# Optimization experiments

Measured on AMD Instinct MI355X. Metric: run time of the kernel, lower is better.

The kernel has to match this reference:

```python
import jax, jax.numpy as jnp
import numpy as np

L, B, H, P = 2048, 16, 512, 256
EPS = 1e-6  # flax nnx LayerNorm default


def setup_inputs() -> dict:
    key = jax.random.key(0)
    ks = jax.random.split(key, 12)
    x = jax.random.normal(ks[0], (L, B, H), jnp.float32)
    d = jax.random.bernoulli(ks[1], 0.01, (L, B))  # sparse reset signal
    hidden_re = jnp.zeros((1, B, P), jnp.float32)
    hidden_im = jnp.zeros((1, B, P), jnp.float32)
    # S5 diagonal state matrix (stable: Re < 0)
    Lambda_re = -0.5 * jnp.exp(0.5 * jax.random.normal(ks[2], (P,), jnp.float32))
    Lambda_im = np.float32(np.pi) * jax.random.normal(ks[3], (P,), jnp.float32)
    B_re = jax.random.normal(ks[4], (P, H), jnp.float32) / np.sqrt(2.0 * H).astype(np.float32)
    B_im = jax.random.normal(ks[5], (P, H), jnp.float32) / np.sqrt(2.0 * H).astype(np.float32)
    C_re = jax.random.normal(ks[6], (H, P), jnp.float32) / np.sqrt(P).astype(np.float32)
    C_im = jax.random.normal(ks[7], (H, P), jnp.float32) / np.sqrt(P).astype(np.float32)
    D = jax.random.normal(ks[8], (H,), jnp.float32)
    log_step = jax.random.uniform(ks[9], (P,), jnp.float32,
                                  minval=np.log(1e-3).astype(np.float32),
                                  maxval=np.log(1e-1).astype(np.float32))
    ln_scale = jnp.ones((H,), jnp.float32)
    ln_bias = jnp.zeros((H,), jnp.float32)
    out2_w = jax.random.normal(ks[10], (H, H), jnp.float32) / np.sqrt(H).astype(np.float32)
    out2_b = jnp.zeros((H,), jnp.float32)
    return dict(x=x, d=d, hidden_re=hidden_re, hidden_im=hidden_im,
                Lambda_re=Lambda_re, Lambda_im=Lambda_im, B_re=B_re, B_im=B_im,
                C_re=C_re, C_im=C_im, D=D, log_step=log_step,
                ln_scale=ln_scale, ln_bias=ln_bias, out2_w=out2_w, out2_b=out2_b)


def reference(x, d, hidden_re, hidden_im, Lambda_re, Lambda_im, B_re, B_im,
              C_re, C_im, D, log_step, ln_scale, ln_bias, out2_w, out2_b):
    def ln(v):
        mu = v.mean(-1, keepdims=True)
        var = v.var(-1, keepdims=True)
        return (v - mu) * jax.lax.rsqrt(var + EPS) * ln_scale + ln_bias

    skip = x
    xn = ln(x)  # prenorm

    # --- S5 SSM (ZOH discretization), vmapped over batch == vectorized over axis 1 ---
    step = jnp.exp(log_step)  # step_rescale = 1.0
    Lam = (Lambda_re + 1j * Lambda_im).astype(jnp.complex64)          # (P,)
    Lam_bar = jnp.exp(Lam * step.astype(jnp.complex64))                # (P,)
    B_bar = ((Lam_bar - 1.0) / Lam)[:, None] * (B_re + 1j * B_im).astype(jnp.complex64)  # (P,H)
    Bu = jnp.einsum('lbh,ph->lbp', xn.astype(jnp.complex64), B_bar)    # (L,B,P)

    keep = (1.0 - d.astype(jnp.float32)).astype(jnp.complex64)         # reset zeroes the carry
    a = Lam_bar[None, None, :] * keep[:, :, None]                      # (L,B,P)
    h0 = (hidden_re + 1j * hidden_im).astype(jnp.complex64)[0]         # (B,P)
    Bu = Bu.at[0].add(a[0] * h0)                                       # fold in initial hidden

    def binop(e1, e2):
        a1, b1 = e1
        a2, b2 = e2
        return (a2 * a1, a2 * b1 + b2)

    _, xs = jax.lax.associative_scan(binop, (a, Bu), axis=0)           # (L,B,P) states
    Cmat = (C_re + 1j * C_im).astype(jnp.complex64)
    ys = 2.0 * jnp.einsum('lbp,hp->lbh', xs, Cmat).real + D * xn       # conj-sym readout + feedthrough
    new_hidden = xs[-1:]                                               # (1,B,P)

    y = ln(ys)  # gtrxl norm (shared LayerNorm)
    # half_glu2: x * sigmoid(W2 gelu(x) + b2)
    x1 = jax.nn.gelu(y)  # approximate=True matches nnx.gelu
    y = y * jax.nn.sigmoid(x1 @ out2_w + out2_b)
    out = skip + y
    return (new_hidden.real, new_hidden.imag, out)
```

## Files before the change

### kernel.cpp

```cpp
#include <hip/hip_runtime.h>

#define LL 2048
#define BB 16
#define HH 512
#define PP 256
#define MM (LL*BB)
#define NN 512
#define KK 512
#define NC 64
#define CLEN 32

typedef __bf16 bf16x8 __attribute__((ext_vector_type(8)));
typedef float  f32x4  __attribute__((ext_vector_type(4)));

__device__ __forceinline__ unsigned short f2bf(float f) {
  unsigned u = __builtin_bit_cast(unsigned, f);
  u = (u + 0x7fffu + ((u >> 16) & 1u)) >> 16;
  return (unsigned short)u;
}
__device__ __forceinline__ float bf2f(unsigned short s) {
  unsigned u = ((unsigned)s) << 16;
  return __builtin_bit_cast(float, u);
}

__global__ void detect_kernel(const unsigned int* __restrict__ dw, int* __restrict__ flag) {
  __shared__ int sInt, sFloat;
  if (threadIdx.x == 0) { sInt = 1; sFloat = 1; }
  __syncthreads();
  int allInt = 1, allFloat = 1;
  for (int i = threadIdx.x; i < 8192; i += 256) {
    unsigned v = dw[i];
    if (v > 1u) allInt = 0;
    if (v != 0u && v != 0x3f800000u) allFloat = 0;
  }
  if (!allInt) atomicAnd(&sInt, 0);
  if (!allFloat) atomicAnd(&sFloat, 0);
  __syncthreads();
  if (threadIdx.x == 0) *flag = sInt ? 0 : (sFloat ? 1 : 2);
}

__device__ __forceinline__ float keep_val(const void* d, int flag, int idx) {
  if (flag == 0) return 1.f - (float)((const int*)d)[idx];
  if (flag == 1) return 1.f - ((const float*)d)[idx];
  return 1.f - (float)((const unsigned char*)d)[idx];
}

__global__ void precompute_kernel(
    const float* __restrict__ Lre, const float* __restrict__ Lim,
    const float* __restrict__ Bre, const float* __restrict__ Bim,
    const float* __restrict__ Cre, const float* __restrict__ Cim,
    const float* __restrict__ lstep, const float* __restrict__ w2,
    unsigned short* __restrict__ W1t, unsigned short* __restrict__ W2t,
    unsigned short* __restrict__ W3t, float* __restrict__ lam_re,
    float* __restrict__ lam_im) {
  int t = blockIdx.x * 256 + threadIdx.x;
  int k = t & (KK - 1);
  int n = t >> 9;
  {
    int p = n & (PP - 1);
    float lr = Lre[p], li = Lim[p];
    float st = expf(lstep[p]);
    float er = expf(lr * st);
    float ang = li * st;
    float lbr = er * cosf(ang), lbi = er * sinf(ang);
    float den = lr * lr + li * li;
    float wr = ((lbr - 1.f) * lr + lbi * li) / den;
    float wi = (lbi * lr - (lbr - 1.f) * li) / den;
    float br = Bre[p * HH + k], bi = Bim[p * HH + k];
    float v = (n < PP) ? (wr * br - wi * bi) : (wr * bi + wi * br);
    W1t[(size_t)n * KK + k] = f2bf(v);
  }
  {
    float v = (k < PP) ? (2.f * Cre[n * PP + k]) : (-2.f * Cim[n * PP + (k - PP)]);
    W2t[(size_t)n * KK + k] = f2bf(v);
  }
  W3t[(size_t)n * KK + k] = f2bf(w2[(size_t)k * HH + n]);
  if (t < PP) {
    float lr = Lre[t], li = Lim[t];
    float st = expf(lstep[t]);
    float er = expf(lr * st);
    float ang = li * st;
    lam_re[t] = er * cosf(ang);
    lam_im[t] = er * sinf(ang);
  }
}

__global__ void ln1_kernel(const float* __restrict__ x, const float* __restrict__ sc,
                           const float* __restrict__ bs, unsigned short* __restrict__ xn) {
  int row = blockIdx.x * 4 + (threadIdx.x >> 6);
  int lane = threadIdx.x & 63;
  const float4* xr = (const float4*)(x + (size_t)row * HH) + lane * 2;
  float4 a = xr[0], b = xr[1];
  float s = (a.x + a.y) + (a.z + a.w) + (b.x + b.y) + (b.z + b.w);
  float q = a.x * a.x + a.y * a.y + a.z * a.z + a.w * a.w +
            b.x * b.x + b.y * b.y + b.z * b.z + b.w * b.w;
#pragma unroll
  for (int off = 32; off; off >>= 1) { s += __shfl_xor(s, off); q += __shfl_xor(q, off); }
  float mean = s * (1.f / HH);
  float var = fmaxf(q * (1.f / HH) - mean * mean, 0.f);
  float rstd = rsqrtf(var + 1e-6f);
  const float4* scp = (const float4*)sc + lane * 2;
  const float4* bsp = (const float4*)bs + lane * 2;
  float4 s0 = scp[0], s1 = scp[1], b0 = bsp[0], b1 = bsp[1];
  unsigned short o[8];
  o[0] = f2bf((a.x - mean) * rstd * s0.x + b0.x);
  o[1] = f2bf((a.y - mean) * rstd * s0.y + b0.y);
  o[2] = f2bf((a.z - mean) * rstd * s0.z + b0.z);
  o[3] = f2bf((a.w - mean) * rstd * s0.w + b0.w);
  o[4] = f2bf((b.x - mean) * rstd * s1.x + b1.x);
  o[5] = f2bf((b.y - mean) * rstd * s1.y + b1.y);
  o[6] = f2bf((b.z - mean) * rstd * s1.z + b1.z);
  o[7] = f2bf((b.w - mean) * rstd * s1.w + b1.w);
  uint4 pk;
  pk.x = o[0] | ((unsigned)o[1] << 16);
  pk.y = o[2] | ((unsigned)o[3] << 16);
  pk.z = o[4] | ((unsigned)o[5] << 16);
  pk.w = o[6] | ((unsigned)o[7] << 16);
  *((uint4*)(xn + (size_t)row * HH) + lane) = pk;
}

__global__ void ln2_kernel(const float* __restrict__ ys, const float* __restrict__ sc,
                           const float* __restrict__ bs, unsigned short* __restrict__ y,
                           unsigned short* __restrict__ x1) {
  int row = blockIdx.x * 4 + (threadIdx.x >> 6);
  int lane = threadIdx.x & 63;
  const float4* xr = (const float4*)(ys + (size_t)row * HH) + lane * 2;
  float4 a = xr[0], b = xr[1];
  float s = (a.x + a.y) + (a.z + a.w) + (b.x + b.y) + (b.z + b.w);
  float q = a.x * a.x + a.y * a.y + a.z * a.z + a.w * a.w +
            b.x * b.x + b.y * b.y + b.z * b.z + b.w * b.w;
#pragma unroll
  for (int off = 32; off; off >>= 1) { s += __shfl_xor(s, off); q += __shfl_xor(q, off); }
  float mean = s * (1.f / HH);
  float var = fmaxf(q * (1.f / HH) - mean * mean, 0.f);
  float rstd = rsqrtf(var + 1e-6f);
  const float4* scp = (const float4*)sc + lane * 2;
  const float4* bsp = (const float4*)bs + lane * 2;
  float4 s0 = scp[0], s1 = scp[1], b0 = bsp[0], b1 = bsp[1];
  float v[8] = { a.x, a.y, a.z, a.w, b.x, b.y, b.z, b.w };
  float scv[8] = { s0.x, s0.y, s0.z, s0.w, s1.x, s1.y, s1.z, s1.w };
  float bsv[8] = { b0.x, b0.y, b0.z, b0.w, b1.x, b1.y, b1.z, b1.w };
  unsigned short oy[8], og[8];
#pragma unroll
  for (int j = 0; j < 8; j++) {
    float yv = (v[j] - mean) * rstd * scv[j] + bsv[j];
    oy[j] = f2bf(yv);
    float g = 0.5f * yv * (1.f + tanhf(0.7978845608f * (yv + 0.044715f * yv * yv * yv)));
    og[j] = f2bf(g);
  }
  uint4 py, pg;
  py.x = oy[0] | ((unsigned)oy[1] << 16); py.y = oy[2] | ((unsigned)oy[3] << 16);
  py.z = oy[4] | ((unsigned)oy[5] << 16); py.w = oy[6] | ((unsigned)oy[7] << 16);
  pg.x = og[0] | ((unsigned)og[1] << 16); pg.y = og[2] | ((unsigned)og[3] << 16);
  pg.z = og[4] | ((unsigned)og[5] << 16); pg.w = og[6] | ((unsigned)og[7] << 16);
  *((uint4*)(y  + (size_t)row * HH) + lane) = py;
  *((uint4*)(x1 + (size_t)row * HH) + lane) = pg;
}

template <int EPI>
__global__ __launch_bounds__(256, 4) void gemm_kernel(
    const unsigned short* __restrict__ A, const unsigned short* __restrict__ Wt,
    float* __restrict__ Cout, const float* __restrict__ Dvec,
    const unsigned short* __restrict__ aux16, const float* __restrict__ skip) {
  __shared__ alignas(16) unsigned short lA[128 * 64];
  __shared__ alignas(16) unsigned short lB[128 * 64];
  int tid = threadIdx.x;
  int w = tid >> 6, lane = tid & 63;
  int wgid = blockIdx.x;
  int xcd = wgid & 7, idx = wgid >> 3;
  int m0 = (xcd * 32 + (idx >> 2)) * 128;
  int n0 = (idx & 3) * 128;
  int wr = w >> 1, wc = w & 1;
  f32x4 acc[4][4];
#pragma unroll
  for (int i = 0; i < 4; i++)
#pragma unroll
    for (int j = 0; j < 4; j++) acc[i][j] = (f32x4){0.f, 0.f, 0.f, 0.f};

  for (int kt = 0; kt < KK / 64; ++kt) {
    __syncthreads();
#pragma unroll
    for (int i = 0; i < 4; i++) {
      int sidx = i * 256 + tid;
      int r = sidx >> 3, c = sidx & 7;
      int cs = c ^ (r & 7);
      const unsigned short* g = A + (size_t)(m0 + r) * KK + kt * 64 + cs * 8;
      unsigned short* l = &lA[(i * 256 + w * 64) * 8];
      __builtin_amdgcn_global_load_lds((const __attribute__((address_space(1))) void*)g,
                                       (__attribute__((address_space(3))) void*)l, 16, 0, 0);
    }
#pragma unroll
    for (int i = 0; i < 4; i++) {
      int sidx = i * 256 + tid;
      int r = sidx >> 3, c = sidx & 7;
      int cs = c ^ (r & 7);
      const unsigned short* g = Wt + (size_t)(n0 + r) * KK + kt * 64 + cs * 8;
      unsigned short* l = &lB[(i * 256 + w * 64) * 8];
      __builtin_amdgcn_global_load_lds((const __attribute__((address_space(1))) void*)g,
                                       (__attribute__((address_space(3))) void*)l, 16, 0, 0);
    }
    __syncthreads();
#pragma unroll
    for (int ks = 0; ks < 2; ++ks) {
      bf16x8 aF[4], bF[4];
#pragma unroll
      for (int m = 0; m < 4; m++) {
        int row = wr * 64 + m * 16 + (lane & 15);
        int s = ks * 4 + (lane >> 4);
        aF[m] = *reinterpret_cast<const bf16x8*>(&lA[row * 64 + (s ^ (row & 7)) * 8]);
      }
#pragma unroll
      for (int n = 0; n < 4; n++) {
        int row = wc * 64 + n * 16 + (lane & 15);
        int s = ks * 4 + (lane >> 4);
        bF[n] = *reinterpret_cast<const bf16x8*>(&lB[row * 64 + (s ^ (row & 7)) * 8]);
      }
#pragma unroll
      for (int m = 0; m < 4; m++)
#pragma unroll
        for (int n = 0; n < 4; n++)
          acc[m][n] = __builtin_amdgcn_mfma_f32_16x16x32_bf16(aF[m], bF[n], acc[m][n], 0, 0, 0);
    }
  }
  int lr4 = (lane >> 4) * 4, lc = lane & 15;
#pragma unroll
  for (int m = 0; m < 4; m++) {
    int rowb = m0 + wr * 64 + m * 16 + lr4;
#pragma unroll
    for (int n = 0; n < 4; n++) {
      int col = n0 + wc * 64 + n * 16 + lc;
#pragma unroll
      for (int j = 0; j < 4; j++) {
        int row = rowb + j;
        size_t idxo = (size_t)row * NN + col;
        float v = acc[m][n][j];
        if (EPI == 0) {
          Cout[idxo] = v;
        } else if (EPI == 1) {
          Cout[idxo] = v + Dvec[col] * bf2f(aux16[idxo]);
        } else {
          float z = v + Dvec[col];
          float sg = 1.f / (1.f + expf(-z));
          Cout[idxo] = skip[idxo] + bf2f(aux16[idxo]) * sg;
        }
      }
    }
  }
}

__global__ void scanA_kernel(const float* __restrict__ Bu, const void* __restrict__ d,
                             const int* __restrict__ dflag, const float* __restrict__ lam_re,
                             const float* __restrict__ lam_im, float* __restrict__ Ar,
                             float* __restrict__ Ai, float* __restrict__ Sr,
                             float* __restrict__ Si) {
  int bx = blockIdx.x;
  int c = bx >> 4, b = bx & 15;
  int p = threadIdx.x;
  int fl = *dflag;
  float lr = lam_re[p], li = lam_im[p];
  float Apr = 1.f, Api = 0.f, sr = 0.f, si = 0.f;
  int l0 = c * CLEN;
  for (int j = 0; j < CLEN; j++) {
    int l = l0 + j;
    float kp = keep_val(d, fl, l * BB + b);
    float ar = lr * kp, ai = li * kp;
    size_t ro = (size_t)(l * BB + b) * NN;
    float bur = Bu[ro + p], bui = Bu[ro + PP + p];
    float nsr = ar * sr - ai * si + bur;
    float nsi = ar * si + ai * sr + bui;
    sr = nsr; si = nsi;
    float nar = ar * Apr - ai * Api;
    float nai = ar * Api + ai * Apr;
    Apr = nar; Api = nai;
  }
  int o = bx * PP + p;
  Ar[o] = Apr; Ai[o] = Api; Sr[o] = sr; Si[o] = si;
}

__global__ void scanB_kernel(const float* __restrict__ hr0, const float* __restrict__ hi0,
                             const float* __restrict__ Ar, const float* __restrict__ Ai,
                             const float* __restrict__ Sr, const float* __restrict__ Si,
                             float* __restrict__ Cr, float* __restrict__ Ci,
                             float* __restrict__ outHid) {
  int b = blockIdx.x;
  int p = threadIdx.x;
  float cr = hr0[b * PP + p], ci = hi0[b * PP + p];
  for (int c = 0; c < NC; c++) {
    int o = (c * BB + b) * PP + p;
    Cr[o] = cr; Ci[o] = ci;
    float ar = Ar[o], ai = Ai[o];
    float nr = ar * cr - ai * ci + Sr[o];
    float ni = ar * ci + ai * cr + Si[o];
    cr = nr; ci = ni;
  }
  outHid[b * PP + p] = cr;
  outHid[BB * PP + b * PP + p] = ci;
}

__global__ void scanC_kernel(const float* __restrict__ Bu, const void* __restrict__ d,
                             const int* __restrict__ dflag, const float* __restrict__ lam_re,
                             const float* __restrict__ lam_im, const float* __restrict__ Cr,
                             const float* __restrict__ Ci, unsigned short* __restrict__ xs) {
  int bx = blockIdx.x;
  int c = bx >> 4, b = bx & 15;
  int p = threadIdx.x;
  int fl = *dflag;
  float lr = lam_re[p], li = lam_im[p];
  float hr = Cr[bx * PP + p], hi = Ci[bx * PP + p];
  int l0 = c * CLEN;
  for (int j = 0; j < CLEN; j++) {
    int l = l0 + j;
    float kp = keep_val(d, fl, l * BB + b);
    float ar = lr * kp, ai = li * kp;
    size_t ro = (size_t)(l * BB + b) * NN;
    float bur = Bu[ro + p], bui = Bu[ro + PP + p];
    float nhr = ar * hr - ai * hi + bur;
    float nhi = ar * hi + ai * hr + bui;
    hr = nhr; hi = nhi;
    xs[ro + p] = f2bf(hr);
    xs[ro + PP + p] = f2bf(hi);
  }
}

extern "C" void kernel_launch(void* const* d_in, const int* in_sizes, int n_in,
                              void* d_out, int out_size, void* d_ws, size_t ws_size,
                              hipStream_t stream) {
  const float* x    = (const float*)d_in[0];
  const void*  dmask= d_in[1];
  const float* hidr = (const float*)d_in[2];
  const float* hidi = (const float*)d_in[3];
  const float* Lre  = (const float*)d_in[4];
  const float* Lim  = (const float*)d_in[5];
  const float* Bre  = (const float*)d_in[6];
  const float* Bim  = (const float*)d_in[7];
  const float* Cre  = (const float*)d_in[8];
  const float* Cim  = (const float*)d_in[9];
  const float* Dv   = (const float*)d_in[10];
  const float* lst  = (const float*)d_in[11];
  const float* lsc  = (const float*)d_in[12];
  const float* lbs  = (const float*)d_in[13];
  const float* w2   = (const float*)d_in[14];
  const float* b2   = (const float*)d_in[15];
  float* out = (float*)d_out;

  char* ws = (char*)d_ws;
  size_t off = 0;
  auto alloc = [&](size_t bytes) -> void* {
    void* p = ws + off;
    off += (bytes + 255) & ~(size_t)255;
    return p;
  };
  unsigned short* xn  = (unsigned short*)alloc((size_t)MM * KK * 2);
  unsigned short* xs  = (unsigned short*)alloc((size_t)MM * KK * 2);
  float* Bu           = (float*)alloc((size_t)MM * NN * 4);
  unsigned short* W1t = (unsigned short*)alloc((size_t)NN * KK * 2);
  unsigned short* W2t = (unsigned short*)alloc((size_t)NN * KK * 2);
  unsigned short* W3t = (unsigned short*)alloc((size_t)NN * KK * 2);
  float* lam_re = (float*)alloc(PP * 4);
  float* lam_im = (float*)alloc(PP * 4);
  float* Ar = (float*)alloc((size_t)NC * BB * PP * 4);
  float* Ai = (float*)alloc((size_t)NC * BB * PP * 4);
  float* Sr = (float*)alloc((size_t)NC * BB * PP * 4);
  float* Si = (float*)alloc((size_t)NC * BB * PP * 4);
  float* Cr = (float*)alloc((size_t)NC * BB * PP * 4);
  float* Ci = (float*)alloc((size_t)NC * BB * PP * 4);
  int* dflag = (int*)alloc(256);
  unsigned short* y  = xn;
  unsigned short* x1 = xs;
  float* ysb = Bu;

  detect_kernel<<<1, 256, 0, stream>>>((const unsigned int*)dmask, dflag);
  precompute_kernel<<<1024, 256, 0, stream>>>(Lre, Lim, Bre, Bim, Cre, Cim, lst, w2,
                                              W1t, W2t, W3t, lam_re, lam_im);
  ln1_kernel<<<MM / 4, 256, 0, stream>>>(x, lsc, lbs, xn);
  gemm_kernel<0><<<1024, 256, 0, stream>>>(xn, W1t, Bu, nullptr, nullptr, nullptr);
  scanA_kernel<<<NC * BB, 256, 0, stream>>>(Bu, dmask, dflag, lam_re, lam_im, Ar, Ai, Sr, Si);
  scanB_kernel<<<BB, 256, 0, stream>>>(hidr, hidi, Ar, Ai, Sr, Si, Cr, Ci, out);
  scanC_kernel<<<NC * BB, 256, 0, stream>>>(Bu, dmask, dflag, lam_re, lam_im, Cr, Ci, xs);
  gemm_kernel<1><<<1024, 256, 0, stream>>>(xs, W2t, ysb, Dv, xn, nullptr);
  ln2_kernel<<<MM / 4, 256, 0, stream>>>(ysb, lsc, lbs, y, x1);
  gemm_kernel<2><<<1024, 256, 0, stream>>>(x1, W3t, out + 2 * BB * PP, b2, y, x);
}
```

Baseline: 221.6 us.

## Store Bu and SSM readout in bf16 and double-buffer GEMM LDS tiles

Switches the intermediate Bu and pre-LayerNorm readout buffers from fp32 to bf16, so the GEMM epilogues, scan kernels and ln2 read and write half the bytes. The GEMM also gains double-buffered LDS staging, issuing the next k-tile's global-to-LDS loads while the current tile is computed, with launch bounds lowered to allow the larger LDS footprint. Rounding Bu to bf16 before the recurrent scan adds accuracy risk, because errors accumulate along the sequence. The doubled LDS use may also reduce occupancy.

```diff
diff --git a/kernel.cpp b/kernel.cpp
--- a/kernel.cpp
+++ b/kernel.cpp
@@ -9,6 +9,7 @@
 #define KK 512
 #define NC 64
 #define CLEN 32
+#define NKT (KK/64)
 
 typedef __bf16 bf16x8 __attribute__((ext_vector_type(8)));
 typedef float  f32x4  __attribute__((ext_vector_type(4)));
@@ -119,16 +120,20 @@
   *((uint4*)(xn + (size_t)row * HH) + lane) = pk;
 }
 
-__global__ void ln2_kernel(const float* __restrict__ ys, const float* __restrict__ sc,
+__global__ void ln2_kernel(const unsigned short* __restrict__ ys, const float* __restrict__ sc,
                            const float* __restrict__ bs, unsigned short* __restrict__ y,
                            unsigned short* __restrict__ x1) {
   int row = blockIdx.x * 4 + (threadIdx.x >> 6);
   int lane = threadIdx.x & 63;
-  const float4* xr = (const float4*)(ys + (size_t)row * HH) + lane * 2;
-  float4 a = xr[0], b = xr[1];
-  float s = (a.x + a.y) + (a.z + a.w) + (b.x + b.y) + (b.z + b.w);
-  float q = a.x * a.x + a.y * a.y + a.z * a.z + a.w * a.w +
-            b.x * b.x + b.y * b.y + b.z * b.z + b.w * b.w;
+  uint4 pin = *((const uint4*)(ys + (size_t)row * HH) + lane);
+  float v[8];
+  v[0] = bf2f((unsigned short)(pin.x & 0xffff)); v[1] = bf2f((unsigned short)(pin.x >> 16));
+  v[2] = bf2f((unsigned short)(pin.y & 0xffff)); v[3] = bf2f((unsigned short)(pin.y >> 16));
+  v[4] = bf2f((unsigned short)(pin.z & 0xffff)); v[5] = bf2f((unsigned short)(pin.z >> 16));
+  v[6] = bf2f((unsigned short)(pin.w & 0xffff)); v[7] = bf2f((unsigned short)(pin.w >> 16));
+  float s = 0.f, q = 0.f;
+#pragma unroll
+  for (int j = 0; j < 8; j++) { s += v[j]; q += v[j] * v[j]; }
 #pragma unroll
   for (int off = 32; off; off >>= 1) { s += __shfl_xor(s, off); q += __shfl_xor(q, off); }
   float mean = s * (1.f / HH);
@@ -137,7 +142,6 @@
   const float4* scp = (const float4*)sc + lane * 2;
   const float4* bsp = (const float4*)bs + lane * 2;
   float4 s0 = scp[0], s1 = scp[1], b0 = bsp[0], b1 = bsp[1];
-  float v[8] = { a.x, a.y, a.z, a.w, b.x, b.y, b.z, b.w };
   float scv[8] = { s0.x, s0.y, s0.z, s0.w, s1.x, s1.y, s1.z, s1.w };
   float bsv[8] = { b0.x, b0.y, b0.z, b0.w, b1.x, b1.y, b1.z, b1.w };
   unsigned short oy[8], og[8];
@@ -158,18 +162,18 @@
 }
 
 template <int EPI>
-__global__ __launch_bounds__(256, 4) void gemm_kernel(
+__global__ __launch_bounds__(256, 2) void gemm_kernel(
     const unsigned short* __restrict__ A, const unsigned short* __restrict__ Wt,
-    float* __restrict__ Cout, const float* __restrict__ Dvec,
+    void* __restrict__ Cout, const float* __restrict__ Dvec,
     const unsigned short* __restrict__ aux16, const float* __restrict__ skip) {
-  __shared__ alignas(16) unsigned short lA[128 * 64];
-  __shared__ alignas(16) unsigned short lB[128 * 64];
+  __shared__ alignas(16) unsigned short lA[2][128 * 64];
+  __shared__ alignas(16) unsigned short lB[2][128 * 64];
   int tid = threadIdx.x;
   int w = tid >> 6, lane = tid & 63;
   int wgid = blockIdx.x;
-  int xcd = wgid & 7, idx = wgid >> 3;
-  int m0 = (xcd * 32 + (idx >> 2)) * 128;
-  int n0 = (idx & 3) * 128;
+  int xcd = wgid & 7, bidx = wgid >> 3;
+  int m0 = (xcd * 32 + (bidx >> 2)) * 128;
+  int n0 = (bidx & 3) * 128;
   int wr = w >> 1, wc = w & 1;
   f32x4 acc[4][4];
 #pragma unroll
@@ -177,15 +181,14 @@
 #pragma unroll
     for (int j = 0; j < 4; j++) acc[i][j] = (f32x4){0.f, 0.f, 0.f, 0.f};
 
-  for (int kt = 0; kt < KK / 64; ++kt) {
-    __syncthreads();
+  auto stage = [&](int buf, int kt) {
 #pragma unroll
     for (int i = 0; i < 4; i++) {
       int sidx = i * 256 + tid;
       int r = sidx >> 3, c = sidx & 7;
       int cs = c ^ (r & 7);
       const unsigned short* g = A + (size_t)(m0 + r) * KK + kt * 64 + cs * 8;
-      unsigned short* l = &lA[(i * 256 + w * 64) * 8];
+      unsigned short* l = &lA[buf][(i * 256 + w * 64) * 8];
       __builtin_amdgcn_global_load_lds((const __attribute__((address_space(1))) void*)g,
                                        (__attribute__((address_space(3))) void*)l, 16, 0, 0);
     }
@@ -195,11 +198,18 @@
       int r = sidx >> 3, c = sidx & 7;
       int cs = c ^ (r & 7);
       const unsigned short* g = Wt + (size_t)(n0 + r) * KK + kt * 64 + cs * 8;
-      unsigned short* l = &lB[(i * 256 + w * 64) * 8];
+      unsigned short* l = &lB[buf][(i * 256 + w * 64) * 8];
       __builtin_amdgcn_global_load_lds((const __attribute__((address_space(1))) void*)g,
                                        (__attribute__((address_space(3))) void*)l, 16, 0, 0);
     }
-    __syncthreads();
+  };
+
+  stage(0, 0);
+  __syncthreads();
+#pragma unroll
+  for (int kt = 0; kt < NKT; ++kt) {
+    int cur = kt & 1;
+    if (kt + 1 < NKT) stage(cur ^ 1, kt + 1);
 #pragma unroll
     for (int ks = 0; ks < 2; ++ks) {
       bf16x8 aF[4], bF[4];
@@ -207,13 +217,13 @@
       for (int m = 0; m < 4; m++) {
         int row = wr * 64 + m * 16 + (lane & 15);
         int s = ks * 4 + (lane >> 4);
-        aF[m] = *reinterpret_cast<const bf16x8*>(&lA[row * 64 + (s ^ (row & 7)) * 8]);
+        aF[m] = *reinterpret_cast<const bf16x8*>(&lA[cur][row * 64 + (s ^ (row & 7)) * 8]);
       }
 #pragma unroll
       for (int n = 0; n < 4; n++) {
         int row = wc * 64 + n * 16 + (lane & 15);
         int s = ks * 4 + (lane >> 4);
-        bF[n] = *reinterpret_cast<const bf16x8*>(&lB[row * 64 + (s ^ (row & 7)) * 8]);
+        bF[n] = *reinterpret_cast<const bf16x8*>(&lB[cur][row * 64 + (s ^ (row & 7)) * 8]);
       }
 #pragma unroll
       for (int m = 0; m < 4; m++)
@@ -221,6 +231,7 @@
         for (int n = 0; n < 4; n++)
           acc[m][n] = __builtin_amdgcn_mfma_f32_16x16x32_bf16(aF[m], bF[n], acc[m][n], 0, 0, 0);
     }
+    __syncthreads();
   }
   int lr4 = (lane >> 4) * 4, lc = lane & 15;
 #pragma unroll
@@ -235,20 +246,20 @@
         size_t idxo = (size_t)row * NN + col;
         float v = acc[m][n][j];
         if (EPI == 0) {
-          Cout[idxo] = v;
+          ((unsigned short*)Cout)[idxo] = f2bf(v);
         } else if (EPI == 1) {
-          Cout[idxo] = v + Dvec[col] * bf2f(aux16[idxo]);
+          ((unsigned short*)Cout)[idxo] = f2bf(v + Dvec[col] * bf2f(aux16[idxo]));
         } else {
           float z = v + Dvec[col];
           float sg = 1.f / (1.f + expf(-z));
-          Cout[idxo] = skip[idxo] + bf2f(aux16[idxo]) * sg;
+          ((float*)Cout)[idxo] = skip[idxo] + bf2f(aux16[idxo]) * sg;
         }
       }
     }
   }
 }
 
-__global__ void scanA_kernel(const float* __restrict__ Bu, const void* __restrict__ d,
+__global__ void scanA_kernel(const unsigned short* __restrict__ Bu, const void* __restrict__ d,
                              const int* __restrict__ dflag, const float* __restrict__ lam_re,
                              const float* __restrict__ lam_im, float* __restrict__ Ar,
                              float* __restrict__ Ai, float* __restrict__ Sr,
@@ -265,7 +276,7 @@
     float kp = keep_val(d, fl, l * BB + b);
     float ar = lr * kp, ai = li * kp;
     size_t ro = (size_t)(l * BB + b) * NN;
-    float bur = Bu[ro + p], bui = Bu[ro + PP + p];
+    float bur = bf2f(Bu[ro + p]), bui = bf2f(Bu[ro + PP + p]);
     float nsr = ar * sr - ai * si + bur;
     float nsi = ar * si + ai * sr + bui;
     sr = nsr; si = nsi;
@@ -297,7 +308,7 @@
   outHid[BB * PP + b * PP + p] = ci;
 }
 
-__global__ void scanC_kernel(const float* __restrict__ Bu, const void* __restrict__ d,
+__global__ void scanC_kernel(const unsigned short* __restrict__ Bu, const void* __restrict__ d,
                              const int* __restrict__ dflag, const float* __restrict__ lam_re,
                              const float* __restrict__ lam_im, const float* __restrict__ Cr,
                              const float* __restrict__ Ci, unsigned short* __restrict__ xs) {
@@ -313,7 +324,7 @@
     float kp = keep_val(d, fl, l * BB + b);
     float ar = lr * kp, ai = li * kp;
     size_t ro = (size_t)(l * BB + b) * NN;
-    float bur = Bu[ro + p], bui = Bu[ro + PP + p];
+    float bur = bf2f(Bu[ro + p]), bui = bf2f(Bu[ro + PP + p]);
     float nhr = ar * hr - ai * hi + bur;
     float nhi = ar * hi + ai * hr + bui;
     hr = nhr; hi = nhi;
@@ -352,7 +363,7 @@
   };
   unsigned short* xn  = (unsigned short*)alloc((size_t)MM * KK * 2);
   unsigned short* xs  = (unsigned short*)alloc((size_t)MM * KK * 2);
-  float* Bu           = (float*)alloc((size_t)MM * NN * 4);
+  unsigned short* Bu  = (unsigned short*)alloc((size_t)MM * NN * 2);
   unsigned short* W1t = (unsigned short*)alloc((size_t)NN * KK * 2);
   unsigned short* W2t = (unsigned short*)alloc((size_t)NN * KK * 2);
   unsigned short* W3t = (unsigned short*)alloc((size_t)NN * KK * 2);
@@ -365,9 +376,9 @@
   float* Cr = (float*)alloc((size_t)NC * BB * PP * 4);
   float* Ci = (float*)alloc((size_t)NC * BB * PP * 4);
   int* dflag = (int*)alloc(256);
-  unsigned short* y  = xn;
-  unsigned short* x1 = xs;
-  float* ysb = Bu;
+  unsigned short* y   = xn;
+  unsigned short* x1  = xs;
+  unsigned short* ysb = Bu;
 
   detect_kernel<<<1, 256, 0, stream>>>((const unsigned int*)dmask, dflag);
   precompute_kernel<<<1024, 256, 0, stream>>>(Lre, Lim, Bre, Bim, Cre, Cim, lst, w2,
```

After: 196.2 us. -11.5%, faster.
